# Optimization experiments

Measured on AMD Instinct MI355X. Metric: run time of the kernel, lower is better.

The kernel has to match this reference:

```python
import jax, jax.numpy as jnp
import numpy as np

B, T, V, E, H, L = 32, 128, 32000, 1024, 1024, 3


def lstm_layer(x, Wx, Wh, b, h0, c0):
    """Standard LSTM (i,f,g,o gate order). x: [B,T,D]. Returns ([B,T,H], (h,c))."""
    def step(carry, xt):
        h, c = carry
        z = xt @ Wx + h @ Wh + b          # [B, 4H]
        i, f, g, o = jnp.split(z, 4, axis=-1)
        c = jax.nn.sigmoid(f) * c + jax.nn.sigmoid(i) * jnp.tanh(g)
        h = jax.nn.sigmoid(o) * jnp.tanh(c)
        return (h, c), h
    (h, c), ys = jax.lax.scan(step, (h0, c0), jnp.swapaxes(x, 0, 1))
    return jnp.swapaxes(ys, 0, 1), (h, c)


def setup_inputs() -> dict:
    key = jax.random.key(0)
    ks = jax.random.split(key, 12)
    s = 0.05  # small init to avoid gate saturation
    inp = {
        "enc_ids": jax.random.randint(ks[0], (B, T), 0, V, dtype=jnp.int32),
        "dec_ids": jax.random.randint(ks[1], (B, T), 0, V, dtype=jnp.int32),
        "emb": jax.random.normal(ks[2], (V, E), jnp.float32) * s,
        "Wx_enc": jax.random.normal(ks[3], (L, E, 4 * H), jnp.float32) * s,
        "Wh_enc": jax.random.normal(ks[4], (L, H, 4 * H), jnp.float32) * s,
        "b_enc": jnp.zeros((L, 4 * H), jnp.float32),
        "Wx_dec": jax.random.normal(ks[5], (L, E, 4 * H), jnp.float32) * s,
        "Wh_dec": jax.random.normal(ks[6], (L, H, 4 * H), jnp.float32) * s,
        "b_dec": jnp.zeros((L, 4 * H), jnp.float32),
        "dense_W": jax.random.normal(ks[7], (H, V), jnp.float32) * s,
        "dense_b": jnp.zeros((V,), jnp.float32),
    }
    return inp


def reference(enc_ids, dec_ids, emb, Wx_enc, Wh_enc, b_enc, Wx_dec, Wh_dec, b_dec, dense_W, dense_b):
    zeros = jnp.zeros((B, H), jnp.float32)
    # encoder: 3 stacked LSTMs, zero initial state each
    x = emb[enc_ids]                                      # [B,T,E]
    state = (zeros, zeros)
    for l in range(L):
        x, state = lstm_layer(x, Wx_enc[l], Wh_enc[l], b_enc[l], zeros, zeros)
    # decoder: faithful to source state chaining:
    # dec layer0 init = enc layer2 final; dec layer_{i+1} init = dec layer_i final
    y = emb[dec_ids]                                      # [B,T,E]
    for l in range(L):
        y, state = lstm_layer(y, Wx_dec[l], Wh_dec[l], b_dec[l], state[0], state[1])
    logits = y.reshape(-1, H) @ dense_W + dense_b          # [B*T, V]
    return logits.reshape(B, T, V)
```

## Files before the change

kernel.cpp:

```cpp
#include <hip/hip_runtime.h>


typedef __bf16 bf8 __attribute__((ext_vector_type(8)));
typedef float  f4  __attribute__((ext_vector_type(4)));

#define TLEN  128
#define HID   1024
#define G4    4096
#define VOC   32000
#define NBLK_SEQ 64

__device__ __forceinline__ ushort f2bf(float f) {
  unsigned u = __builtin_bit_cast(unsigned, f);
  u += 0x7fffu + ((u >> 16) & 1u);
  return (ushort)(u >> 16);
}
__device__ __forceinline__ float sigmoidf_(float x) { return 1.f / (1.f + expf(-x)); }

__device__ __forceinline__ void ld16_sys(uint4& v, const void* p) {
  asm volatile("global_load_dwordx4 %0, %1, off sc0 sc1" : "=v"(v) : "v"(p));
}
__device__ __forceinline__ unsigned ld4_sys(const void* p) {
  unsigned v;
  asm volatile("global_load_dword %0, %1, off sc0 sc1\n\ts_waitcnt vmcnt(0)"
               : "=v"(v) : "v"(p) : "memory");
  return v;
}
__device__ __forceinline__ void ld4_sys3(unsigned& a, unsigned& b, unsigned& c,
                                         const void* pa, const void* pb, const void* pc) {
  asm volatile("global_load_dword %0, %3, off sc0 sc1\n\t"
               "global_load_dword %1, %4, off sc0 sc1\n\t"
               "global_load_dword %2, %5, off sc0 sc1\n\t"
               "s_waitcnt vmcnt(0)"
               : "=&v"(a), "=&v"(b), "=&v"(c)
               : "v"(pa), "v"(pb), "v"(pc) : "memory");
}
__device__ __forceinline__ void st4_sys(void* p, unsigned v) {
  asm volatile("global_store_dword %0, %1, off sc0 sc1" :: "v"(p), "v"(v) : "memory");
}
__device__ __forceinline__ void wait_vm0() {
  asm volatile("s_waitcnt vmcnt(0)" ::: "memory");
  __builtin_amdgcn_sched_barrier(0);
}

typedef const __attribute__((address_space(1))) void GvoidC;
typedef __attribute__((address_space(3))) void Lvoid;
__device__ __forceinline__ void g2l16(const void* g, void* l) {
  __builtin_amdgcn_global_load_lds((GvoidC*)g, (Lvoid*)l, 16, 0, 0);
}

__global__ __launch_bounds__(256) void embed_kernel(const int* __restrict__ ids,
    const float* __restrict__ emb, ushort* __restrict__ out) {
  int r = blockIdx.x;
  int b = r & 31, t = r >> 5;
  int id = ids[b * TLEN + t];
  const float4* src = (const float4*)(emb + (size_t)id * HID);
  float4 v = src[threadIdx.x];
  ushort4 o;
  o.x = f2bf(v.x); o.y = f2bf(v.y); o.z = f2bf(v.z); o.w = f2bf(v.w);
  *(ushort4*)(out + (size_t)r * HID + threadIdx.x * 4) = o;
}

__global__ __launch_bounds__(256) void transpose_cvt(const float* __restrict__ W,
    ushort* __restrict__ Wt, int R, int C) {
  __shared__ float tile[32][33];
  int tx = threadIdx.x & 31, ty = threadIdx.x >> 5;
  int c0 = blockIdx.x * 32, r0 = blockIdx.y * 32;
  #pragma unroll
  for (int i = 0; i < 32; i += 8)
    tile[ty + i][tx] = W[(size_t)(r0 + ty + i) * C + c0 + tx];
  __syncthreads();
  #pragma unroll
  for (int i = 0; i < 32; i += 8)
    Wt[(size_t)(c0 + ty + i) * R + r0 + tx] = f2bf(tile[tx][ty + i]);
}

__global__ __launch_bounds__(256) void gemm_bt(const ushort* __restrict__ A,
    const ushort* __restrict__ Bt, const float* __restrict__ bias,
    float* __restrict__ C, int M, int N, int K, int permute) {
  __shared__ __align__(16) ushort lA[128 * 32];
  __shared__ __align__(16) ushort lB[128 * 32];
  int tid = threadIdx.x;
  int lane = tid & 63, wave = tid >> 6;
  int nwg = gridDim.x * gridDim.y;
  int wg  = blockIdx.y * gridDim.x + blockIdx.x;
  int q   = nwg >> 3;
  int swg = (wg & 7) * q + (wg >> 3);
  int m0 = (swg / gridDim.x) * 128, n0 = (swg % gridDim.x) * 128;
  int wr = wave >> 1, wc = wave & 1;
  f4 zero = {0.f, 0.f, 0.f, 0.f};
  f4 acc[4][4];
  #pragma unroll
  for (int i = 0; i < 4; i++)
    #pragma unroll
    for (int j = 0; j < 4; j++) acc[i][j] = zero;

  const ushort* Ag = A  + (size_t)(m0 + wave * 32 + (lane >> 2)) * K + (lane & 3) * 8;
  const ushort* Bg = Bt + (size_t)(n0 + wave * 32 + (lane >> 2)) * K + (lane & 3) * 8;
  ushort* lAp = lA + wave * 32 * 32;
  ushort* lBp = lB + wave * 32 * 32;

  for (int kt = 0; kt < K; kt += 32) {
    g2l16(Ag + kt, lAp);
    g2l16(Ag + (size_t)16 * K + kt, lAp + 16 * 32);
    g2l16(Bg + kt, lBp);
    g2l16(Bg + (size_t)16 * K + kt, lBp + 16 * 32);
    __syncthreads();
    bf8 aF[4], bF[4];
    #pragma unroll
    for (int i = 0; i < 4; i++)
      aF[i] = *(const bf8*)(lA + (wr * 64 + i * 16 + (lane & 15)) * 32 + (lane >> 4) * 8);
    #pragma unroll
    for (int j = 0; j < 4; j++)
      bF[j] = *(const bf8*)(lB + (wc * 64 + j * 16 + (lane & 15)) * 32 + (lane >> 4) * 8);
    #pragma unroll
    for (int i = 0; i < 4; i++)
      #pragma unroll
      for (int j = 0; j < 4; j++)
        acc[i][j] = __builtin_amdgcn_mfma_f32_16x16x32_bf16(aF[i], bF[j], acc[i][j], 0, 0, 0);
    __syncthreads();
  }
  #pragma unroll
  for (int i = 0; i < 4; i++) {
    #pragma unroll
    for (int j = 0; j < 4; j++) {
      int col = n0 + wc * 64 + j * 16 + (lane & 15);
      float bv = bias ? bias[col] : 0.f;
      #pragma unroll
      for (int v = 0; v < 4; v++) {
        int row = m0 + wr * 64 + i * 16 + (lane >> 4) * 4 + v;
        int orow = permute ? ((row & 31) * TLEN + (row >> 5)) : row;
        C[(size_t)orow * N + col] = acc[i][j][v] + bv;
      }
    }
  }
}

__global__ __launch_bounds__(512, 1) void enc_wave(
    const float*  __restrict__ Zpre,
    const ushort* __restrict__ WhT,
    const ushort* __restrict__ WxT,
    const float*  __restrict__ bE,
    ushort*       __restrict__ hxC,
    float*        __restrict__ cSe,
    ushort*       __restrict__ hS,
    unsigned*     __restrict__ flags)
{
  const int bx = blockIdx.x;
  const int l = bx >> 6, jg = bx & 63;
  const int j0 = jg * 16;
  const int tid = threadIdx.x;
  const int lane = tid & 63, wave = tid >> 6;
  const int op = wave >> 2, ks = wave & 3;
  const int rr = tid >> 4, jj = tid & 15;

  __shared__ float zp[8][4][32][17];

  float cc = cSe[(size_t)l * 32768 + rr * HID + j0 + jj];
  float bias4[4];
  #pragma unroll
  for (int g = 0; g < 4; g++)
    bias4[g] = bE[l * G4 + g * HID + j0 + jj];

  const bool mfma_on = (l > 0) || (op == 0);
  bf8 bw[4][8];
  if (mfma_on) {
    const ushort* Wb = op ? (WxT + (size_t)(l - 1) * G4 * HID)
                          : (WhT + (size_t)l * G4 * HID);
    #pragma unroll
    for (int g = 0; g < 4; g++) {
      const ushort* Bp = Wb + (size_t)(g * HID + j0 + (lane & 15)) * HID
                       + ks * 256 + (lane >> 4) * 8;
      #pragma unroll
      for (int kk = 0; kk < 8; kk++)
        bw[g][kk] = *(const bf8*)(Bp + kk * 32);
    }
  }

  const int r0 = lane & 15, r1 = r0 + 16;
  const int lk = lane >> 4;
  const int aoff0 = ks * 8192 + (lk >> 1) * 512 + r0 * 16 + (lk & 1) * 8;
  const int aoff1 = ks * 8192 + (lk >> 1) * 512 + r1 * 16 + (lk & 1) * 8;

  float zv4[4], zn4[4];
  if (l == 0) {
    #pragma unroll
    for (int g = 0; g < 4; g++)
      zv4[g] = Zpre[(size_t)rr * G4 + g * HID + j0 + jj];
  }

  for (int w = 0; w < 130; ++w) {
    if (w > 0) {
      if (wave == 0) {
        for (;;) {
          unsigned a, b, c;
          ld4_sys3(a, b, c, flags + lane * 4, flags + (64 + lane) * 4,
                   flags + (128 + lane) * 4);
          if (!__ballot(a < (unsigned)w || b < (unsigned)w || c < (unsigned)w)) break;
          __builtin_amdgcn_s_sleep(1);
        }
      }
      __syncthreads();
    }
    const int t = w - l;
    if (t >= 0 && t < TLEN) {
      uint4 ha0[8], ha1[8];
      if (mfma_on) {
        const ushort* src = (op == 0)
          ? hxC + ((size_t)l * 2 + ((t - 1) & 1)) * 32768
          : hxC + ((size_t)(l - 1) * 2 + (t & 1)) * 32768;
        #pragma unroll
        for (int kk = 0; kk < 8; kk++) {
          ld16_sys(ha0[kk], src + aoff0 + kk * 1024);
          ld16_sys(ha1[kk], src + aoff1 + kk * 1024);
        }
        wait_vm0();
      }

      if (l == 0 && t + 1 < TLEN) {
        const float* Ztn = Zpre + (size_t)(t + 1) * 32 * G4;
        #pragma unroll
        for (int g = 0; g < 4; g++)
          zn4[g] = Ztn[(size_t)rr * G4 + g * HID + j0 + jj];
      }

      if (mfma_on) {
        f4 acc0[4], acc1[4];
        #pragma unroll
        for (int g = 0; g < 4; g++) { acc0[g] = (f4){0,0,0,0}; acc1[g] = (f4){0,0,0,0}; }
        #pragma unroll
        for (int kk = 0; kk < 8; kk++) {
          bf8 a0 = __builtin_bit_cast(bf8, ha0[kk]);
          bf8 a1 = __builtin_bit_cast(bf8, ha1[kk]);
          #pragma unroll
          for (int g = 0; g < 4; g++) {
            acc0[g] = __builtin_amdgcn_mfma_f32_16x16x32_bf16(a0, bw[g][kk], acc0[g], 0, 0, 0);
            acc1[g] = __builtin_amdgcn_mfma_f32_16x16x32_bf16(a1, bw[g][kk], acc1[g], 0, 0, 0);
          }
        }
        #pragma unroll
        for (int g = 0; g < 4; g++)
          #pragma unroll
          for (int v = 0; v < 4; v++) {
            zp[wave][g][(lane >> 4) * 4 + v][lane & 15]      = acc0[g][v];
            zp[wave][g][16 + (lane >> 4) * 4 + v][lane & 15] = acc1[g][v];
          }
      }
      __syncthreads();

      float z[4];
      #pragma unroll
      for (int g = 0; g < 4; g++) {
        float s = zp[0][g][rr][jj] + zp[1][g][rr][jj]
                + zp[2][g][rr][jj] + zp[3][g][rr][jj];
        if (l > 0)
          s += zp[4][g][rr][jj] + zp[5][g][rr][jj]
             + zp[6][g][rr][jj] + zp[7][g][rr][jj] + bias4[g];
        else
          s += zv4[g];
        z[g] = s;
      }
      if (l == 0) {
        #pragma unroll
        for (int g = 0; g < 4; g++) zv4[g] = zn4[g];
      }
      float ig = sigmoidf_(z[0]), fg = sigmoidf_(z[1]);
      float gv = tanhf(z[2]),     og = sigmoidf_(z[3]);
      cc = fg * cc + ig * gv;
      float hv = og * tanhf(cc);
      ushort hb = f2bf(hv);
      unsigned u = (unsigned)hb;
      unsigned nb = __shfl_xor(u, 1);
      if ((jj & 1) == 0)
        st4_sys(hxC + ((size_t)l * 2 + (t & 1)) * 32768 + jg * 512 + rr * 16 + jj,
                u | (nb << 16));
      if (t == TLEN - 1) {
        hS [(size_t)l * 32768 + rr * HID + j0 + jj] = hb;
        cSe[(size_t)l * 32768 + rr * HID + j0 + jj] = cc;
      }
      wait_vm0();
    }
    __syncthreads();
    if (tid == 0) st4_sys(flags + bx * 4, (unsigned)(w + 1));
  }
}

__global__ __launch_bounds__(256, 1) void lstm_seq(
    const float*  __restrict__ Zpre,
    const ushort* __restrict__ Wht,
    float*        __restrict__ cS,
    ushort*       __restrict__ yout,
    ushort*       __restrict__ hx,
    unsigned*     __restrict__ flags)
{
  const int jg = blockIdx.x;
  const int j0 = jg * 16;
  const int tid = threadIdx.x;
  const int lane = tid & 63, wave = tid >> 6;
  const int rr = tid >> 3, cp = tid & 7;

  __shared__ float zp[4][4][32][17];

  float2 cc = *(const float2*)(cS + (size_t)rr * HID + j0 + 2 * cp);

  bf8 bw[4][8];
  #pragma unroll
  for (int g = 0; g < 4; g++) {
    const ushort* Bp = Wht + (size_t)(g * HID + j0 + (lane & 15)) * HID
                     + wave * 256 + (lane >> 4) * 8;
    #pragma unroll
    for (int kk = 0; kk < 8; kk++)
      bw[g][kk] = *(const bf8*)(Bp + kk * 32);
  }

  const int r0 = lane & 15, r1 = r0 + 16;
  const int lk = lane >> 4;
  const int aoff0 = wave * 8192 + (lk >> 1) * 512 + r0 * 16 + (lk & 1) * 8;
  const int aoff1 = wave * 8192 + (lk >> 1) * 512 + r1 * 16 + (lk & 1) * 8;

  float2 zv[4], zn[4];
  #pragma unroll
  for (int g = 0; g < 4; g++)
    zv[g] = *(const float2*)(Zpre + (size_t)rr * G4 + g * HID + j0 + 2 * cp);

  for (int t = 0; t < TLEN; ++t) {
    if (t > 0) {
      if (wave == 0) {
        const unsigned* fp = flags + lane * 4;
        while (__ballot(ld4_sys(fp) < (unsigned)t)) __builtin_amdgcn_s_sleep(1);
      }
      __syncthreads();
    }
    const ushort* hsrc = hx + ((t + 1) & 1) * 32768;
    uint4 ha0[8], ha1[8];
    #pragma unroll
    for (int kk = 0; kk < 8; kk++) {
      ld16_sys(ha0[kk], hsrc + aoff0 + kk * 1024);
      ld16_sys(ha1[kk], hsrc + aoff1 + kk * 1024);
    }
    wait_vm0();

    if (t + 1 < TLEN) {
      const float* Ztn = Zpre + (size_t)(t + 1) * 32 * G4;
      #pragma unroll
      for (int g = 0; g < 4; g++)
        zn[g] = *(const float2*)(Ztn + (size_t)rr * G4 + g * HID + j0 + 2 * cp);
    }

    f4 acc0[4], acc1[4];
    #pragma unroll
    for (int g = 0; g < 4; g++) { acc0[g] = (f4){0,0,0,0}; acc1[g] = (f4){0,0,0,0}; }
    #pragma unroll
    for (int kk = 0; kk < 8; kk++) {
      bf8 a0 = __builtin_bit_cast(bf8, ha0[kk]);
      bf8 a1 = __builtin_bit_cast(bf8, ha1[kk]);
      #pragma unroll
      for (int g = 0; g < 4; g++) {
        acc0[g] = __builtin_amdgcn_mfma_f32_16x16x32_bf16(a0, bw[g][kk], acc0[g], 0, 0, 0);
        acc1[g] = __builtin_amdgcn_mfma_f32_16x16x32_bf16(a1, bw[g][kk], acc1[g], 0, 0, 0);
      }
    }
    #pragma unroll
    for (int g = 0; g < 4; g++)
      #pragma unroll
      for (int v = 0; v < 4; v++) {
        zp[wave][g][(lane >> 4) * 4 + v][lane & 15]      = acc0[g][v];
        zp[wave][g][16 + (lane >> 4) * 4 + v][lane & 15] = acc1[g][v];
      }
    __syncthreads();

    float zx[4], zy[4];
    #pragma unroll
    for (int g = 0; g < 4; g++) {
      zx[g] = zv[g].x + zp[0][g][rr][2 * cp]     + zp[1][g][rr][2 * cp]
                      + zp[2][g][rr][2 * cp]     + zp[3][g][rr][2 * cp];
      zy[g] = zv[g].y + zp[0][g][rr][2 * cp + 1] + zp[1][g][rr][2 * cp + 1]
                      + zp[2][g][rr][2 * cp + 1] + zp[3][g][rr][2 * cp + 1];
    }
    cc.x = sigmoidf_(zx[1]) * cc.x + sigmoidf_(zx[0]) * tanhf(zx[2]);
    cc.y = sigmoidf_(zy[1]) * cc.y + sigmoidf_(zy[0]) * tanhf(zy[2]);
    float hv0 = sigmoidf_(zx[3]) * tanhf(cc.x);
    float hv1 = sigmoidf_(zy[3]) * tanhf(cc.y);
    unsigned packed = (unsigned)f2bf(hv0) | ((unsigned)f2bf(hv1) << 16);
    *(unsigned*)(yout + (size_t)t * 32768 + rr * HID + j0 + 2 * cp) = packed;
    st4_sys(hx + (size_t)(t & 1) * 32768 + jg * 512 + rr * 16 + 2 * cp, packed);
    #pragma unroll
    for (int g = 0; g < 4; g++) zv[g] = zn[g];

    wait_vm0();
    __syncthreads();
    if (tid == 0) st4_sys(flags + jg * 4, (unsigned)(t + 1));
  }
  *(float2*)(cS + (size_t)rr * HID + j0 + 2 * cp) = cc;
}

__global__ __launch_bounds__(256) void prep_enc(ushort* hxC, float* cSe,
                                                unsigned* flags) {
  int i = blockIdx.x * 256 + threadIdx.x;
  hxC[i] = 0;
  if (i < 98304) cSe[i] = 0.f;
  if (i < 192)   flags[i * 4] = 0;
}
__global__ __launch_bounds__(256) void prep_dec0(const ushort* __restrict__ hS2,
                                                 const float* __restrict__ cSe2,
                                                 float* cS, ushort* hx,
                                                 unsigned* flags) {
  int i = blockIdx.x * 256 + threadIdx.x;
  int row = i >> 10, col = i & 1023;
  hx[32768 + (col >> 4) * 512 + row * 16 + (col & 15)] = hS2[i];
  cS[i] = cSe2[i];
  if (i < NBLK_SEQ) flags[i * 4] = 0;
}
__global__ __launch_bounds__(256) void prep_copy(const ushort* __restrict__ src,
                                                 ushort* __restrict__ hx,
                                                 unsigned* __restrict__ flags) {
  int i = blockIdx.x * 256 + threadIdx.x;
  int row = i >> 10, col = i & 1023;
  hx[32768 + (col >> 4) * 512 + row * 16 + (col & 15)] = src[i];
  if (i < NBLK_SEQ) flags[i * 4] = 0;
}

extern "C" void kernel_launch(void* const* d_in, const int* in_sizes, int n_in,
                              void* d_out, int out_size, void* d_ws, size_t ws_size,
                              hipStream_t stream) {
  const int*   enc_ids = (const int*)d_in[0];
  const int*   dec_ids = (const int*)d_in[1];
  const float* emb     = (const float*)d_in[2];
  const float* Wx_enc  = (const float*)d_in[3];
  const float* Wh_enc  = (const float*)d_in[4];
  const float* b_enc   = (const float*)d_in[5];
  const float* Wx_dec  = (const float*)d_in[6];
  const float* Wh_dec  = (const float*)d_in[7];
  const float* b_dec   = (const float*)d_in[8];
  const float* dense_W = (const float*)d_in[9];
  const float* dense_b = (const float*)d_in[10];
  float* out = (float*)d_out;

  char* ws = (char*)d_ws;
  const size_t SZ_BUF = (size_t)4096 * 1024 * 2;
  ushort*   bufA   = (ushort*)(ws);
  ushort*   bufB   = (ushort*)(ws + SZ_BUF);
  ushort*   Wxt    = (ushort*)(ws + 2 * SZ_BUF);
  ushort*   Wht    = (ushort*)(ws + 3 * SZ_BUF);
  ushort*   dWt    = (ushort*)(ws + 4 * SZ_BUF);
  char*     p2     = ws + 4 * SZ_BUF + (size_t)VOC * 1024 * 2;
  float*    cS     = (float*)(p2 + (size_t)32 * 1024 * 2);
  unsigned* flags  = (unsigned*)(p2 + (size_t)32 * 1024 * 2 + (size_t)32 * 1024 * 4);

  char* ob = (char*)d_out;
  float*    Zpre   = out;
  ushort*   WhTe   = (ushort*)(ob + (size_t)64  * 1024 * 1024);
  ushort*   WxTe   = (ushort*)(ob + (size_t)88  * 1024 * 1024);
  char*     st     = ob + (size_t)112 * 1024 * 1024;
  ushort*   hxC    = (ushort*)st;
  float*    cSe    = (float*)(st + 393216);
  ushort*   hS     = (ushort*)(st + 786432);
  unsigned* flags2 = (unsigned*)(st + 983040);
  ushort*   hxD    = (ushort*)(ob + (size_t)120 * 1024 * 1024);
  const size_t WSTRIDE = (size_t)G4 * HID;

  transpose_cvt<<<dim3(VOC / 32, 1024 / 32), 256, 0, stream>>>(dense_W, dWt, 1024, VOC);

  embed_kernel<<<4096, 256, 0, stream>>>(enc_ids, emb, bufA);
  transpose_cvt<<<dim3(G4 / 32, 32), 256, 0, stream>>>(Wx_enc, Wxt, 1024, G4);
  gemm_bt<<<dim3(G4 / 128, 4096 / 128), 256, 0, stream>>>(bufA, Wxt, b_enc,
                                                          Zpre, 4096, G4, 1024, 0);
  for (int l = 0; l < 3; l++)
    transpose_cvt<<<dim3(G4 / 32, 32), 256, 0, stream>>>(Wh_enc + (size_t)l * 1024 * G4,
                                                         WhTe + l * WSTRIDE, 1024, G4);
  for (int l = 1; l < 3; l++)
    transpose_cvt<<<dim3(G4 / 32, 32), 256, 0, stream>>>(Wx_enc + (size_t)l * 1024 * G4,
                                                         WxTe + (l - 1) * WSTRIDE, 1024, G4);
  prep_enc<<<768, 256, 0, stream>>>(hxC, cSe, flags2);
  enc_wave<<<192, 512, 0, stream>>>(Zpre, WhTe, WxTe, b_enc, hxC, cSe, hS, flags2);

  embed_kernel<<<4096, 256, 0, stream>>>(dec_ids, emb, bufA);
  ushort* cur = bufA; ushort* oth = bufB;
  for (int l = 0; l < 3; l++) {
    transpose_cvt<<<dim3(G4 / 32, 32), 256, 0, stream>>>(Wx_dec + (size_t)l * 1024 * G4, Wxt, 1024, G4);
    transpose_cvt<<<dim3(G4 / 32, 32), 256, 0, stream>>>(Wh_dec + (size_t)l * 1024 * G4, Wht, 1024, G4);
    gemm_bt<<<dim3(G4 / 128, 4096 / 128), 256, 0, stream>>>(cur, Wxt, b_dec + (size_t)l * G4,
                                                            Zpre, 4096, G4, 1024, 0);
    if (l == 0) {
      prep_dec0<<<128, 256, 0, stream>>>(hS + 2 * 32768, cSe + 2 * 32768, cS, hxD, flags);
    } else {
      const ushort* h0src = cur + (size_t)127 * 32 * HID;
      prep_copy<<<128, 256, 0, stream>>>(h0src, hxD, flags);
    }
    lstm_seq<<<NBLK_SEQ, 256, 0, stream>>>(Zpre, Wht, cS, oth, hxD, flags);
    ushort* tmp = cur; cur = oth; oth = tmp;
  }

  gemm_bt<<<dim3(VOC / 128, 4096 / 128), 256, 0, stream>>>(cur, dWt, dense_b, out,
                                                           4096, VOC, 1024, 1);
}
```

Before: 3.160 ms.

## Spin per-wave on step flags, chain decoder flags, double the GEMM K-step

The recurrent kernels now have every wave poll the inter-block step flags directly, with no sleep. This removes the wave-0 poll followed by __syncthreads on each timestep. In enc_wave, only waves that run MFMA poll. The decoder layers use a monotonically increasing flag base, so the prep_copy launch that copied the previous layer's final h into the state buffer is dropped and the state left in place by the prior layer is reused. The gemm_bt kernel also loads two 32-wide K tiles per barrier, halving the barrier count at the cost of doubled LDS use. Busy spinning without sleep can add memory traffic, and the removed block barrier relies on the reduced ordering still being correct.

```diff
diff --git a/kernel.cpp b/kernel.cpp
--- a/kernel.cpp
+++ b/kernel.cpp
@@ -78,8 +78,8 @@
 __global__ __launch_bounds__(256) void gemm_bt(const ushort* __restrict__ A,
     const ushort* __restrict__ Bt, const float* __restrict__ bias,
     float* __restrict__ C, int M, int N, int K, int permute) {
-  __shared__ __align__(16) ushort lA[128 * 32];
-  __shared__ __align__(16) ushort lB[128 * 32];
+  __shared__ __align__(16) ushort lA[2 * 128 * 32];
+  __shared__ __align__(16) ushort lB[2 * 128 * 32];
   int tid = threadIdx.x;
   int lane = tid & 63, wave = tid >> 6;
   int nwg = gridDim.x * gridDim.y;
@@ -97,27 +97,38 @@
 
   const ushort* Ag = A  + (size_t)(m0 + wave * 32 + (lane >> 2)) * K + (lane & 3) * 8;
   const ushort* Bg = Bt + (size_t)(n0 + wave * 32 + (lane >> 2)) * K + (lane & 3) * 8;
-  ushort* lAp = lA + wave * 32 * 32;
-  ushort* lBp = lB + wave * 32 * 32;
-
-  for (int kt = 0; kt < K; kt += 32) {
-    g2l16(Ag + kt, lAp);
-    g2l16(Ag + (size_t)16 * K + kt, lAp + 16 * 32);
-    g2l16(Bg + kt, lBp);
-    g2l16(Bg + (size_t)16 * K + kt, lBp + 16 * 32);
+  ushort* lApa = lA + wave * 1024;
+  ushort* lApb = lA + 4096 + wave * 1024;
+  ushort* lBpa = lB + wave * 1024;
+  ushort* lBpb = lB + 4096 + wave * 1024;
+
+  for (int kt = 0; kt < K; kt += 64) {
+    g2l16(Ag + kt,                    lApa);
+    g2l16(Ag + (size_t)16 * K + kt,       lApa + 512);
+    g2l16(Ag + kt + 32,               lApb);
+    g2l16(Ag + (size_t)16 * K + kt + 32,  lApb + 512);
+    g2l16(Bg + kt,                    lBpa);
+    g2l16(Bg + (size_t)16 * K + kt,       lBpa + 512);
+    g2l16(Bg + kt + 32,               lBpb);
+    g2l16(Bg + (size_t)16 * K + kt + 32,  lBpb + 512);
     __syncthreads();
-    bf8 aF[4], bF[4];
-    #pragma unroll
-    for (int i = 0; i < 4; i++)
-      aF[i] = *(const bf8*)(lA + (wr * 64 + i * 16 + (lane & 15)) * 32 + (lane >> 4) * 8);
-    #pragma unroll
-    for (int j = 0; j < 4; j++)
-      bF[j] = *(const bf8*)(lB + (wc * 64 + j * 16 + (lane & 15)) * 32 + (lane >> 4) * 8);
-    #pragma unroll
-    for (int i = 0; i < 4; i++)
+    #pragma unroll
+    for (int h = 0; h < 2; h++) {
+      const ushort* ab = lA + h * 4096;
+      const ushort* bb = lB + h * 4096;
+      bf8 aF[4], bF[4];
+      #pragma unroll
+      for (int i = 0; i < 4; i++)
+        aF[i] = *(const bf8*)(ab + (wr * 64 + i * 16 + (lane & 15)) * 32 + (lane >> 4) * 8);
       #pragma unroll
       for (int j = 0; j < 4; j++)
-        acc[i][j] = __builtin_amdgcn_mfma_f32_16x16x32_bf16(aF[i], bF[j], acc[i][j], 0, 0, 0);
+        bF[j] = *(const bf8*)(bb + (wc * 64 + j * 16 + (lane & 15)) * 32 + (lane >> 4) * 8);
+      #pragma unroll
+      for (int i = 0; i < 4; i++)
+        #pragma unroll
+        for (int j = 0; j < 4; j++)
+          acc[i][j] = __builtin_amdgcn_mfma_f32_16x16x32_bf16(aF[i], bF[j], acc[i][j], 0, 0, 0);
+    }
     __syncthreads();
   }
   #pragma unroll
@@ -190,17 +201,13 @@
   }
 
   for (int w = 0; w < 130; ++w) {
-    if (w > 0) {
-      if (wave == 0) {
-        for (;;) {
-          unsigned a, b, c;
-          ld4_sys3(a, b, c, flags + lane * 4, flags + (64 + lane) * 4,
-                   flags + (128 + lane) * 4);
-          if (!__ballot(a < (unsigned)w || b < (unsigned)w || c < (unsigned)w)) break;
-          __builtin_amdgcn_s_sleep(1);
-        }
-      }
-      __syncthreads();
+    if (w > 0 && mfma_on) {
+      for (;;) {
+        unsigned a, b, c;
+        ld4_sys3(a, b, c, flags + lane * 4, flags + (64 + lane) * 4,
+                 flags + (128 + lane) * 4);
+        if (!__ballot(a < (unsigned)w || b < (unsigned)w || c < (unsigned)w)) break;
+      }
     }
     const int t = w - l;
     if (t >= 0 && t < TLEN) {
@@ -291,7 +298,8 @@
     float*        __restrict__ cS,
     ushort*       __restrict__ yout,
     ushort*       __restrict__ hx,
-    unsigned*     __restrict__ flags)
+    unsigned*     __restrict__ flags,
+    unsigned fbase)
 {
   const int jg = blockIdx.x;
   const int j0 = jg * 16;
@@ -325,11 +333,9 @@
 
   for (int t = 0; t < TLEN; ++t) {
     if (t > 0) {
-      if (wave == 0) {
-        const unsigned* fp = flags + lane * 4;
-        while (__ballot(ld4_sys(fp) < (unsigned)t)) __builtin_amdgcn_s_sleep(1);
-      }
-      __syncthreads();
+      const unsigned* fp = flags + lane * 4;
+      const unsigned want = fbase + (unsigned)t;
+      while (__ballot(ld4_sys(fp) < want)) {}
     }
     const ushort* hsrc = hx + ((t + 1) & 1) * 32768;
     uint4 ha0[8], ha1[8];
@@ -389,7 +395,7 @@
 
     wait_vm0();
     __syncthreads();
-    if (tid == 0) st4_sys(flags + jg * 4, (unsigned)(t + 1));
+    if (tid == 0) st4_sys(flags + jg * 4, fbase + (unsigned)(t + 1));
   }
   *(float2*)(cS + (size_t)rr * HID + j0 + 2 * cp) = cc;
 }
@@ -409,14 +415,6 @@
   int row = i >> 10, col = i & 1023;
   hx[32768 + (col >> 4) * 512 + row * 16 + (col & 15)] = hS2[i];
   cS[i] = cSe2[i];
-  if (i < NBLK_SEQ) flags[i * 4] = 0;
-}
-__global__ __launch_bounds__(256) void prep_copy(const ushort* __restrict__ src,
-                                                 ushort* __restrict__ hx,
-                                                 unsigned* __restrict__ flags) {
-  int i = blockIdx.x * 256 + threadIdx.x;
-  int row = i >> 10, col = i & 1023;
-  hx[32768 + (col >> 4) * 512 + row * 16 + (col & 15)] = src[i];
   if (i < NBLK_SEQ) flags[i * 4] = 0;
 }
 
@@ -481,13 +479,10 @@
     transpose_cvt<<<dim3(G4 / 32, 32), 256, 0, stream>>>(Wh_dec + (size_t)l * 1024 * G4, Wht, 1024, G4);
     gemm_bt<<<dim3(G4 / 128, 4096 / 128), 256, 0, stream>>>(cur, Wxt, b_dec + (size_t)l * G4,
                                                             Zpre, 4096, G4, 1024, 0);
-    if (l == 0) {
+    if (l == 0)
       prep_dec0<<<128, 256, 0, stream>>>(hS + 2 * 32768, cSe + 2 * 32768, cS, hxD, flags);
-    } else {
-      const ushort* h0src = cur + (size_t)127 * 32 * HID;
-      prep_copy<<<128, 256, 0, stream>>>(h0src, hxD, flags);
-    }
-    lstm_seq<<<NBLK_SEQ, 256, 0, stream>>>(Zpre, Wht, cS, oth, hxD, flags);
+    lstm_seq<<<NBLK_SEQ, 256, 0, stream>>>(Zpre, Wht, cS, oth, hxD, flags,
+                                           (unsigned)(l * TLEN));
     ushort* tmp = cur; cur = oth; oth = tmp;
   }
 
```

Result: no change. 3.134 ms (-0.8%).
